# Kernel optimization log

Measured on AMD Instinct MI355X. Metric: run time of the kernel, lower is better.

The kernel has to match this reference:

```python
import jax, jax.numpy as jnp
import numpy as np

N_NODES = 50000
N_EDGES = 800000
D = 128
ALPHA = 0.2  # LeakyReLU negative slope


def setup_inputs() -> dict:
    key = jax.random.key(0)
    k1, k2, k3, k4 = jax.random.split(key, 4)
    inputs = jax.random.normal(k1, (N_NODES, D), dtype=jnp.float32)
    edge = jax.random.randint(k2, (2, N_EDGES), 0, N_NODES, dtype=jnp.int64)
    # xavier_normal with gain=1.414 as in the torch module
    std_W = 1.414 * np.sqrt(2.0 / (D + D))
    W = jax.random.normal(k3, (D, D), dtype=jnp.float32) * std_W
    std_a = 1.414 * np.sqrt(2.0 / (1 + D))
    a = jax.random.normal(k4, (1, D), dtype=jnp.float32) * std_a
    return {"inputs": inputs, "edge": edge, "W": W, "a": a}


def reference(inputs, edge, W, a):
    # h = inputs @ W  (shared projection; note concat([W,W],0) applied to
    # [x_src || x_dst] is exactly h[src] + h[dst])
    h = inputs @ W                                   # [N, D]
    src, dst = edge[0], edge[1]
    s = h[src] + h[dst]                              # [E, D] gathered edge features
    s = jnp.where(s > 0, s, ALPHA * s)               # LeakyReLU
    edge_e = jnp.exp(s @ a[0])                       # [E] unnormalized attention
    n = inputs.shape[0]
    # sparse.mm(coo, ones) -> per-row sum of edge_e; duplicates summed (coalesce)
    e_rowsum = jax.ops.segment_sum(edge_e, src, num_segments=n)        # [N]
    # sparse.mm(coo, h) -> sum_j edge_e * h[dst]
    h_prime = jax.ops.segment_sum(edge_e[:, None] * h[dst], src, num_segments=n)  # [N, D]
    h_prime = h_prime / e_rowsum[:, None]
    return jax.nn.relu(h_prime)  # concat=True path
```

## Files before the change

### kernel.cpp

```cpp
#include <hip/hip_runtime.h>
#include <cstdint>
#include <cstddef>

#define D 128
#define ALPHA 0.2f

typedef __attribute__((ext_vector_type(8))) short short8_t;
typedef __attribute__((ext_vector_type(4))) float f32x4_t;

static __device__ __forceinline__ ushort f2bf(float f) {
    union { float f; uint32_t u; } v; v.f = f;
    uint32_t r = (v.u + 0x7FFFu + ((v.u >> 16) & 1u)) >> 16;
    return (ushort)r;
}

__global__ __launch_bounds__(256) void w_prep_kernel(const float* __restrict__ W,
                                                     ushort* __restrict__ Wt) {
    int idx = blockIdx.x * 256 + threadIdx.x;
    int k = idx >> 7;
    int n = idx & 127;
    Wt[n * 128 + k] = f2bf(W[idx]);
}

__global__ __launch_bounds__(256) void gemm_h_kernel(const float* __restrict__ A,
                                                     const ushort* __restrict__ Wt,
                                                     ushort* __restrict__ Hb,
                                                     int N) {
    __shared__ ushort Alds[64][136];
    const int tid = threadIdx.x;
    const int r0 = blockIdx.x * 64;

#pragma unroll
    for (int it = 0; it < 8; ++it) {
        int idx = it * 256 + tid;
        int r = idx >> 5;
        int c4 = (idx & 31) * 4;
        float4 v = make_float4(0.f, 0.f, 0.f, 0.f);
        if (r0 + r < N) v = *(const float4*)(A + (size_t)(r0 + r) * D + c4);
        ushort4 b;
        b.x = f2bf(v.x); b.y = f2bf(v.y); b.z = f2bf(v.z); b.w = f2bf(v.w);
        *(ushort4*)&Alds[r][c4] = b;
    }
    __syncthreads();

    const int lane = tid & 63;
    const int w = tid >> 6;
    const int wm = w >> 1;
    const int wn = w & 1;
    const int l15 = lane & 15;
    const int koff = (lane >> 4) * 8;

    f32x4_t acc[2][4];
#pragma unroll
    for (int mt = 0; mt < 2; ++mt)
#pragma unroll
        for (int nt = 0; nt < 4; ++nt) acc[mt][nt] = (f32x4_t){0.f, 0.f, 0.f, 0.f};

    const int arow = wm * 32 + l15;
#pragma unroll
    for (int kk = 0; kk < 4; ++kk) {
        short8_t am0 = *(const short8_t*)&Alds[arow][kk * 32 + koff];
        short8_t am1 = *(const short8_t*)&Alds[arow + 16][kk * 32 + koff];
        short8_t bn[4];
#pragma unroll
        for (int nt = 0; nt < 4; ++nt)
            bn[nt] = *(const short8_t*)(Wt + (size_t)(wn * 64 + nt * 16 + l15) * 128 + kk * 32 + koff);
#pragma unroll
        for (int nt = 0; nt < 4; ++nt) {
            acc[0][nt] = __builtin_amdgcn_mfma_f32_16x16x32_bf16(am0, bn[nt], acc[0][nt], 0, 0, 0);
            acc[1][nt] = __builtin_amdgcn_mfma_f32_16x16x32_bf16(am1, bn[nt], acc[1][nt], 0, 0, 0);
        }
    }

    const int crow = (lane >> 4) * 4;
#pragma unroll
    for (int mt = 0; mt < 2; ++mt)
#pragma unroll
        for (int nt = 0; nt < 4; ++nt)
#pragma unroll
            for (int r = 0; r < 4; ++r) {
                int row = r0 + wm * 32 + mt * 16 + crow + r;
                if (row < N)
                    Hb[(size_t)row * D + wn * 64 + nt * 16 + l15] = f2bf(acc[mt][nt][r]);
            }
}

__global__ __launch_bounds__(256) void hist_rank_kernel(const int* __restrict__ src,
                                                        int* __restrict__ counts,
                                                        int* __restrict__ rank, int E) {
    int i = blockIdx.x * 256 + threadIdx.x;
    if (i >= E) return;
    rank[i] = atomicAdd(&counts[src[i]], 1);
}

__global__ __launch_bounds__(256) void scan_partial_kernel(const int* __restrict__ counts,
                                                           int* __restrict__ blocksum, int N) {
    __shared__ int wsum[4];
    int tid = threadIdx.x;
    int i = blockIdx.x * 256 + tid;
    int x = (i < N) ? counts[i] : 0;
#pragma unroll
    for (int off = 32; off > 0; off >>= 1) x += __shfl_down(x, off);
    if ((tid & 63) == 0) wsum[tid >> 6] = x;
    __syncthreads();
    if (tid == 0) blocksum[blockIdx.x] = wsum[0] + wsum[1] + wsum[2] + wsum[3];
}

__global__ __launch_bounds__(256) void scan_top_kernel(const int* __restrict__ blocksum,
                                                       int* __restrict__ blockoff, int nblk) {
    __shared__ int wsum[4];
    int tid = threadIdx.x;
    int lane = tid & 63, w = tid >> 6;
    int v = (tid < nblk) ? blocksum[tid] : 0;
    int x = v;
#pragma unroll
    for (int off = 1; off < 64; off <<= 1) {
        int y = __shfl_up(x, off);
        if (lane >= off) x += y;
    }
    if (lane == 63) wsum[w] = x;
    __syncthreads();
    int woff = 0;
    for (int i = 0; i < w; ++i) woff += wsum[i];
    if (tid < nblk) blockoff[tid] = woff + x - v;
}

__global__ __launch_bounds__(256) void scan_final_kernel(const int* __restrict__ counts,
                                                         const int* __restrict__ blockoff,
                                                         int* __restrict__ starts, int N) {
    __shared__ int wsum[4];
    int tid = threadIdx.x;
    int lane = tid & 63, w = tid >> 6;
    int i = blockIdx.x * 256 + tid;
    int c = (i < N) ? counts[i] : 0;
    int x = c;
#pragma unroll
    for (int off = 1; off < 64; off <<= 1) {
        int y = __shfl_up(x, off);
        if (lane >= off) x += y;
    }
    if (lane == 63) wsum[w] = x;
    __syncthreads();
    int woff = blockoff[blockIdx.x];
    for (int j = 0; j < w; ++j) woff += wsum[j];
    int pre = woff + x - c;
    if (i < N) {
        starts[i] = pre;
        if (i == N - 1) starts[N] = pre + c;
    }
}

__global__ __launch_bounds__(256) void scatter_kernel(const int* __restrict__ src,
                                                      const int* __restrict__ dst,
                                                      const int* __restrict__ rank,
                                                      const int* __restrict__ starts,
                                                      int* __restrict__ dsts_sorted, int E) {
    int i = blockIdx.x * 256 + threadIdx.x;
    if (i >= E) return;
    int pos = starts[src[i]] + rank[i];
    dsts_sorted[pos] = dst[i];
}

template <bool FULL>
__device__ __forceinline__ void process_chunk(const ushort* __restrict__ Hb,
                                              const int* __restrict__ dsts_sorted,
                                              int base, int cnt, int l,
                                              float hs0, float hs1, float2 av,
                                              int rb, bool wr, float* lds_e,
                                              float& acc0, float& acc1, float& rs) {
    uint fu[16];
#pragma unroll
    for (int j = 0; j < 16; ++j) {
        int idx = FULL ? (base + j) : (base + (j < cnt ? j : 0));
        int dj = dsts_sorted[idx];
        const ushort* rp = Hb + ((size_t)(uint)dj << 7);
        fu[j] = *(const uint*)(rp + (l << 1));
    }
    float p[16];
#pragma unroll
    for (int j = 0; j < 16; ++j) {
        float f0 = __uint_as_float(fu[j] << 16);
        float f1 = __uint_as_float(fu[j] & 0xffff0000u);
        float s0 = hs0 + f0, s1 = hs1 + f1;
        s0 = fmaxf(s0, ALPHA * s0);
        s1 = fmaxf(s1, ALPHA * s1);
        float pj = fmaf(s0, av.x, s1 * av.y);
        p[j] = (FULL || j < cnt) ? pj : -1e30f;
    }
    {
        bool hi = l & 1;
#pragma unroll
        for (int i = 0; i < 8; ++i) {
            float send = hi ? p[i] : p[i + 8];
            float recv = __shfl_xor(send, 1);
            p[i] = (hi ? p[i + 8] : p[i]) + recv;
        }
        hi = l & 2;
#pragma unroll
        for (int i = 0; i < 4; ++i) {
            float send = hi ? p[i] : p[i + 4];
            float recv = __shfl_xor(send, 2);
            p[i] = (hi ? p[i + 4] : p[i]) + recv;
        }
        hi = l & 4;
#pragma unroll
        for (int i = 0; i < 2; ++i) {
            float send = hi ? p[i] : p[i + 2];
            float recv = __shfl_xor(send, 4);
            p[i] = (hi ? p[i + 2] : p[i]) + recv;
        }
        hi = l & 8;
        {
            float send = hi ? p[0] : p[1];
            float recv = __shfl_xor(send, 8);
            p[0] = (hi ? p[1] : p[0]) + recv;
        }
        p[0] += __shfl_xor(p[0], 16);
        p[0] += __shfl_xor(p[0], 32);
    }
    float e = __expf(p[0]);
    if (wr) lds_e[rb] = e;
    __syncthreads();
    float4 e0 = *(const float4*)&lds_e[0];
    float4 e1 = *(const float4*)&lds_e[4];
    float4 e2 = *(const float4*)&lds_e[8];
    float4 e3 = *(const float4*)&lds_e[12];
    __syncthreads();
    float ev[16] = {e0.x, e0.y, e0.z, e0.w, e1.x, e1.y, e1.z, e1.w,
                    e2.x, e2.y, e2.z, e2.w, e3.x, e3.y, e3.z, e3.w};
#pragma unroll
    for (int j = 0; j < 16; ++j) {
        float f0 = __uint_as_float(fu[j] << 16);
        float f1 = __uint_as_float(fu[j] & 0xffff0000u);
        acc0 = fmaf(ev[j], f0, acc0);
        acc1 = fmaf(ev[j], f1, acc1);
        rs += ev[j];
    }
}

__global__ __launch_bounds__(64) void node_kernel(const ushort* __restrict__ Hb,
                                                  const int* __restrict__ starts,
                                                  const int* __restrict__ dsts_sorted,
                                                  const float* __restrict__ a,
                                                  float* __restrict__ out, int N) {
    __shared__ __align__(16) float lds_e[16];
    const int node = blockIdx.x;
    const int l = threadIdx.x;

    const int beg = starts[node];
    const int end = starts[node + 1];

    const ushort* hrow = Hb + ((size_t)node << 7);
    uint hu = *(const uint*)(hrow + (l << 1));
    float hs0 = __uint_as_float(hu << 16);
    float hs1 = __uint_as_float(hu & 0xffff0000u);
    float2 av = *(const float2*)(a + (l << 1));

    const int rb = ((l & 1) << 3) | ((l & 2) << 1) | ((l & 4) >> 1) | ((l & 8) >> 3);
    const bool wr = (l < 16);

    float acc0 = 0.f, acc1 = 0.f, rs = 0.f;

    int base = beg;
    for (; base + 16 <= end; base += 16)
        process_chunk<true>(Hb, dsts_sorted, base, 16, l, hs0, hs1, av, rb, wr,
                            lds_e, acc0, acc1, rs);
    if (base < end)
        process_chunk<false>(Hb, dsts_sorted, base, end - base, l, hs0, hs1, av, rb, wr,
                             lds_e, acc0, acc1, rs);

    float inv = 1.0f / rs;
    float2 o;
    o.x = fmaxf(acc0 * inv, 0.f);
    o.y = fmaxf(acc1 * inv, 0.f);
    *(float2*)(out + ((size_t)node << 7) + (l << 1)) = o;
}

extern "C" void kernel_launch(void* const* d_in, const int* in_sizes, int n_in,
                              void* d_out, int out_size, void* d_ws, size_t ws_size,
                              hipStream_t stream) {
    const float* inputs = (const float*)d_in[0];
    const int* edge = (const int*)d_in[1];
    const float* W = (const float*)d_in[2];
    const float* a = (const float*)d_in[3];
    float* out = (float*)d_out;

    const int N = in_sizes[0] / D;
    const int E = in_sizes[1] / 2;

    const int* src = edge;
    const int* dst = edge + E;

    ushort* wt = (ushort*)d_ws;
    ushort* hb = wt + 128 * 128;
    int* counts = (int*)(hb + (size_t)N * D);
    int* starts = counts + N;
    int* blocksum = starts + N + 1;
    int* blockoff = blocksum + 256;
    int* rank = blockoff + 256;
    int* dsts_sorted = rank + E;

    const int nblk = (N + 255) / 256;
    const int eblk = (E + 255) / 256;

    hipMemsetAsync(counts, 0, (size_t)N * sizeof(int), stream);

    w_prep_kernel<<<64, 256, 0, stream>>>(W, wt);
    gemm_h_kernel<<<(N + 63) / 64, 256, 0, stream>>>(inputs, wt, hb, N);
    hist_rank_kernel<<<eblk, 256, 0, stream>>>(src, counts, rank, E);
    scan_partial_kernel<<<nblk, 256, 0, stream>>>(counts, blocksum, N);
    scan_top_kernel<<<1, 256, 0, stream>>>(blocksum, blockoff, nblk);
    scan_final_kernel<<<nblk, 256, 0, stream>>>(counts, blockoff, starts, N);
    scatter_kernel<<<eblk, 256, 0, stream>>>(src, dst, rank, starts, dsts_sorted, E);
    node_kernel<<<N, 64, 0, stream>>>(hb, starts, dsts_sorted, a, out, N);
}
```

Baseline: 119.5 us.

## Broadcast attention weights via readlane and pack four nodes per block

```diff
diff --git a/kernel.cpp b/kernel.cpp
--- a/kernel.cpp
+++ b/kernel.cpp
@@ -12,6 +12,11 @@
     union { float f; uint32_t u; } v; v.f = f;
     uint32_t r = (v.u + 0x7FFFu + ((v.u >> 16) & 1u)) >> 16;
     return (ushort)r;
+}
+
+__global__ __launch_bounds__(256) void zero_kernel(int* __restrict__ counts, int N) {
+    int i = blockIdx.x * 256 + threadIdx.x;
+    if (i < N) counts[i] = 0;
 }
 
 __global__ __launch_bounds__(256) void w_prep_kernel(const float* __restrict__ W,
@@ -166,7 +171,6 @@
                                               const int* __restrict__ dsts_sorted,
                                               int base, int cnt, int l,
                                               float hs0, float hs1, float2 av,
-                                              int rb, bool wr, float* lds_e,
                                               float& acc0, float& acc1, float& rs) {
     uint fu[16];
 #pragma unroll
@@ -219,33 +223,34 @@
         p[0] += __shfl_xor(p[0], 32);
     }
     float e = __expf(p[0]);
-    if (wr) lds_e[rb] = e;
-    __syncthreads();
-    float4 e0 = *(const float4*)&lds_e[0];
-    float4 e1 = *(const float4*)&lds_e[4];
-    float4 e2 = *(const float4*)&lds_e[8];
-    float4 e3 = *(const float4*)&lds_e[12];
-    __syncthreads();
-    float ev[16] = {e0.x, e0.y, e0.z, e0.w, e1.x, e1.y, e1.z, e1.w,
-                    e2.x, e2.y, e2.z, e2.w, e3.x, e3.y, e3.z, e3.w};
+
+    float rsum = e;
+    rsum += __shfl_xor(rsum, 1);
+    rsum += __shfl_xor(rsum, 2);
+    rsum += __shfl_xor(rsum, 4);
+    rsum += __shfl_xor(rsum, 8);
+    rs += rsum;
+
+    const int brev[16] = {0, 8, 4, 12, 2, 10, 6, 14, 1, 9, 5, 13, 3, 11, 7, 15};
 #pragma unroll
     for (int j = 0; j < 16; ++j) {
+        float ej = __uint_as_float(
+            (uint)__builtin_amdgcn_readlane((int)__float_as_uint(e), brev[j]));
         float f0 = __uint_as_float(fu[j] << 16);
         float f1 = __uint_as_float(fu[j] & 0xffff0000u);
-        acc0 = fmaf(ev[j], f0, acc0);
-        acc1 = fmaf(ev[j], f1, acc1);
-        rs += ev[j];
-    }
-}
-
-__global__ __launch_bounds__(64) void node_kernel(const ushort* __restrict__ Hb,
-                                                  const int* __restrict__ starts,
-                                                  const int* __restrict__ dsts_sorted,
-                                                  const float* __restrict__ a,
-                                                  float* __restrict__ out, int N) {
-    __shared__ __align__(16) float lds_e[16];
-    const int node = blockIdx.x;
-    const int l = threadIdx.x;
+        acc0 = fmaf(ej, f0, acc0);
+        acc1 = fmaf(ej, f1, acc1);
+    }
+}
+
+__global__ __launch_bounds__(256) void node_kernel(const ushort* __restrict__ Hb,
+                                                   const int* __restrict__ starts,
+                                                   const int* __restrict__ dsts_sorted,
+                                                   const float* __restrict__ a,
+                                                   float* __restrict__ out, int N) {
+    const int node = (blockIdx.x << 2) + (threadIdx.x >> 6);
+    if (node >= N) return;
+    const int l = threadIdx.x & 63;
 
     const int beg = starts[node];
     const int end = starts[node + 1];
@@ -256,18 +261,13 @@
     float hs1 = __uint_as_float(hu & 0xffff0000u);
     float2 av = *(const float2*)(a + (l << 1));
 
-    const int rb = ((l & 1) << 3) | ((l & 2) << 1) | ((l & 4) >> 1) | ((l & 8) >> 3);
-    const bool wr = (l < 16);
-
     float acc0 = 0.f, acc1 = 0.f, rs = 0.f;
 
     int base = beg;
     for (; base + 16 <= end; base += 16)
-        process_chunk<true>(Hb, dsts_sorted, base, 16, l, hs0, hs1, av, rb, wr,
-                            lds_e, acc0, acc1, rs);
+        process_chunk<true>(Hb, dsts_sorted, base, 16, l, hs0, hs1, av, acc0, acc1, rs);
     if (base < end)
-        process_chunk<false>(Hb, dsts_sorted, base, end - base, l, hs0, hs1, av, rb, wr,
-                             lds_e, acc0, acc1, rs);
+        process_chunk<false>(Hb, dsts_sorted, base, end - base, l, hs0, hs1, av, acc0, acc1, rs);
 
     float inv = 1.0f / rs;
     float2 o;
@@ -303,8 +303,7 @@
     const int nblk = (N + 255) / 256;
     const int eblk = (E + 255) / 256;
 
-    hipMemsetAsync(counts, 0, (size_t)N * sizeof(int), stream);
-
+    zero_kernel<<<nblk, 256, 0, stream>>>(counts, N);
     w_prep_kernel<<<64, 256, 0, stream>>>(W, wt);
     gemm_h_kernel<<<(N + 63) / 64, 256, 0, stream>>>(inputs, wt, hb, N);
     hist_rank_kernel<<<eblk, 256, 0, stream>>>(src, counts, rank, E);
@@ -312,5 +311,5 @@
     scan_top_kernel<<<1, 256, 0, stream>>>(blocksum, blockoff, nblk);
     scan_final_kernel<<<nblk, 256, 0, stream>>>(counts, blockoff, starts, N);
     scatter_kernel<<<eblk, 256, 0, stream>>>(src, dst, rank, starts, dsts_sorted, E);
-    node_kernel<<<N, 64, 0, stream>>>(hb, starts, dsts_sorted, a, out, N);
-}
+    node_kernel<<<(N + 3) / 4, 256, 0, stream>>>(hb, starts, dsts_sorted, a, out, N);
+}
```

New measurement: 150.9 us. 1.26x slower.
